# Performance work log

Measured on AMD Instinct MI355X. Metric: run time of the kernel, lower is better.

## Reference

```python
import jax, jax.numpy as jnp
import numpy as np

B, N, M = 512, 1024, 128
OUT_DIM, MOLVEC_DIM, IN_DIM = 256, 256, 512


def setup_inputs() -> dict:
    key = jax.random.key(0)
    ks = jax.random.split(key, 6)
    X = jax.random.normal(ks[0], (B, N, OUT_DIM), dtype=jnp.float32)
    molvec = jax.random.normal(ks[1], (B, MOLVEC_DIM), dtype=jnp.float32)
    idx_M = jax.random.randint(ks[2], (B, M), 0, N, dtype=jnp.int64)
    # Xavier-normal-ish scaled linear weights (torch layout: [out_features, in_features])
    fan_in1 = MOLVEC_DIM + OUT_DIM
    W1 = jax.random.normal(ks[3], (IN_DIM, fan_in1), dtype=jnp.float32) * jnp.sqrt(2.0 / (fan_in1 + IN_DIM))
    b1 = jnp.zeros((IN_DIM,), dtype=jnp.float32)
    W2 = jax.random.normal(ks[4], (IN_DIM, IN_DIM), dtype=jnp.float32) * jnp.sqrt(2.0 / (IN_DIM + IN_DIM))
    b2 = jnp.zeros((IN_DIM,), dtype=jnp.float32)
    return {"X": X, "molvec": molvec, "idx_M": idx_M, "W1": W1, "b1": b1, "W2": W2, "b2": b2}


def reference(X, molvec, idx_M, W1, b1, W2, b2):
    # Batched gather: replaces the per-sample index_select loop. [B, M, OUT_DIM]
    target_x = jnp.take_along_axis(X, idx_M[:, :, None], axis=1)
    # Broadcast molvec to each masked position and concat. [B, M, OUT_DIM+MOLVEC_DIM]
    mv = jnp.broadcast_to(molvec[:, None, :], (X.shape[0], idx_M.shape[1], molvec.shape[-1]))
    concat_x = jnp.concatenate([target_x, mv], axis=-1)
    # 2-layer MLP (fc1 -> relu -> fc2)
    h = jax.nn.relu(jnp.einsum('bmd,id->bmi', concat_x, W1) + b1)
    pred = jnp.einsum('bmi,oi->bmo', h, W2) + b2
    return pred.reshape(X.shape[0] * idx_M.shape[1], -1)
```

## Files before the change

kernel.cpp:

```cpp
#include <hip/hip_runtime.h>
#include <hip/hip_bf16.h>

#define BB 512
#define NN 1024
#define MM 128
#define OUTD 256
#define MOLD 256
#define IND 512
#define K1 512
#define RROWS 65536

typedef float f32x4 __attribute__((ext_vector_type(4)));
typedef short s16x8 __attribute__((ext_vector_type(8)));
typedef __bf16 bf16x8 __attribute__((ext_vector_type(8)));

#define AS_GLOBAL const __attribute__((address_space(1))) void
#define AS_LDS __attribute__((address_space(3))) void

__device__ __forceinline__ unsigned short f2bf(float f) {
    unsigned int u = __builtin_bit_cast(unsigned int, f);
    u = (u + 0x7fffu + ((u >> 16) & 1u)) >> 16;
    return (unsigned short)u;
}

__global__ __launch_bounds__(256) void prep_weights(
    const float* __restrict__ W1, const float* __restrict__ W2,
    unsigned short* __restrict__ W1b, unsigned short* __restrict__ W2b) {
    int i = blockIdx.x * 256 + threadIdx.x;
    float4 a = ((const float4*)W1)[i];
    ushort4 pa;
    pa.x = f2bf(a.x); pa.y = f2bf(a.y); pa.z = f2bf(a.z); pa.w = f2bf(a.w);
    ((ushort4*)W1b)[i] = pa;
    float4 b = ((const float4*)W2)[i];
    ushort4 pb;
    pb.x = f2bf(b.x); pb.y = f2bf(b.y); pb.z = f2bf(b.z); pb.w = f2bf(b.w);
    ((ushort4*)W2b)[i] = pb;
}

__global__ __launch_bounds__(256) void gemm1_kernel(
    const float* __restrict__ X, const float* __restrict__ mol,
    const int* __restrict__ idxp, const unsigned short* __restrict__ W1b,
    const float* __restrict__ b1, unsigned short* __restrict__ H) {
    __shared__ __align__(16) unsigned short Asm[128 * 32];
    __shared__ __align__(16) unsigned short Bsm[128 * 32];

    const int t = threadIdx.x;
    const int lane = t & 63, w = t >> 6;
    const int b = blockIdx.x;
    const int n0 = blockIdx.y * 128;
    const int wr = (w >> 1) * 64, wc = (w & 1) * 64;
    const int lr = lane & 15, quad = lane >> 4;

    const int arow = t >> 1;
    const int acol = (t & 1) * 16;
    const int idx = idxp[b * MM + arow];
    const float* Xrow = X + ((size_t)b * NN + idx) * OUTD;
    const float* mvrow = mol + (size_t)b * MOLD;

    f32x4 acc[4][4];
#pragma unroll
    for (int mi = 0; mi < 4; ++mi)
#pragma unroll
        for (int ni = 0; ni < 4; ++ni) acc[mi][ni] = {0.f, 0.f, 0.f, 0.f};

    for (int ki = 0; ki < 16; ++ki) {
        const int kt = ki * 32;
        const float* src = (kt < OUTD) ? (Xrow + kt + acol) : (mvrow + (kt - OUTD) + acol);
        const float4* s4 = (const float4*)src;
        float4 v0 = s4[0], v1 = s4[1], v2 = s4[2], v3 = s4[3];
        unsigned short* dst = &Asm[arow * 32 + acol];
        ushort4 p;
        p.x = f2bf(v0.x); p.y = f2bf(v0.y); p.z = f2bf(v0.z); p.w = f2bf(v0.w);
        *(ushort4*)(dst + 0) = p;
        p.x = f2bf(v1.x); p.y = f2bf(v1.y); p.z = f2bf(v1.z); p.w = f2bf(v1.w);
        *(ushort4*)(dst + 4) = p;
        p.x = f2bf(v2.x); p.y = f2bf(v2.y); p.z = f2bf(v2.z); p.w = f2bf(v2.w);
        *(ushort4*)(dst + 8) = p;
        p.x = f2bf(v3.x); p.y = f2bf(v3.y); p.z = f2bf(v3.z); p.w = f2bf(v3.w);
        *(ushort4*)(dst + 12) = p;
#pragma unroll
        for (int j = 0; j < 2; ++j) {
            const int cidx = j * 4 + w;
            const int s = cidx * 64 + lane;
            const unsigned short* gb = W1b + (size_t)(n0 + (s >> 2)) * K1 + kt + (s & 3) * 8;
            __builtin_amdgcn_global_load_lds((AS_GLOBAL*)gb, (AS_LDS*)(Bsm + cidx * 512), 16, 0, 0);
        }
        __syncthreads();
        s16x8 af[4], bfr[4];
#pragma unroll
        for (int i = 0; i < 4; ++i)
            af[i] = *(const s16x8*)&Asm[(wr + i * 16 + lr) * 32 + quad * 8];
#pragma unroll
        for (int i = 0; i < 4; ++i)
            bfr[i] = *(const s16x8*)&Bsm[(wc + i * 16 + lr) * 32 + quad * 8];
#pragma unroll
        for (int mi = 0; mi < 4; ++mi)
#pragma unroll
            for (int ni = 0; ni < 4; ++ni)
                acc[mi][ni] = __builtin_amdgcn_mfma_f32_16x16x32_bf16(
                    __builtin_bit_cast(bf16x8, af[mi]),
                    __builtin_bit_cast(bf16x8, bfr[ni]), acc[mi][ni], 0, 0, 0);
        __syncthreads();
    }

    float bias[4];
#pragma unroll
    for (int ni = 0; ni < 4; ++ni) bias[ni] = b1[n0 + wc + ni * 16 + lr];
    const int row0 = b * 128;
#pragma unroll
    for (int mi = 0; mi < 4; ++mi) {
#pragma unroll
        for (int ni = 0; ni < 4; ++ni) {
            const int gcol = n0 + wc + ni * 16 + lr;
#pragma unroll
            for (int rr = 0; rr < 4; ++rr) {
                const int grow = row0 + wr + mi * 16 + quad * 4 + rr;
                float v = acc[mi][ni][rr] + bias[ni];
                v = v > 0.f ? v : 0.f;
                H[(size_t)grow * IND + gcol] = f2bf(v);
            }
        }
    }
}

__global__ __launch_bounds__(256) void gemm2_kernel(
    const unsigned short* __restrict__ Hb, const unsigned short* __restrict__ W2b,
    const float* __restrict__ b2, float* __restrict__ out) {
    __shared__ __align__(16) unsigned short Asm[128 * 32];
    __shared__ __align__(16) unsigned short Bsm[128 * 32];

    const int t = threadIdx.x;
    const int lane = t & 63, w = t >> 6;
    const int row0 = blockIdx.x * 128;
    const int n0 = blockIdx.y * 128;
    const int wr = (w >> 1) * 64, wc = (w & 1) * 64;
    const int lr = lane & 15, quad = lane >> 4;

    f32x4 acc[4][4];
#pragma unroll
    for (int mi = 0; mi < 4; ++mi)
#pragma unroll
        for (int ni = 0; ni < 4; ++ni) acc[mi][ni] = {0.f, 0.f, 0.f, 0.f};

    for (int ki = 0; ki < 16; ++ki) {
        const int kt = ki * 32;
#pragma unroll
        for (int j = 0; j < 2; ++j) {
            const int cidx = j * 4 + w;
            const int s = cidx * 64 + lane;
            const unsigned short* ga = Hb + (size_t)(row0 + (s >> 2)) * IND + kt + (s & 3) * 8;
            __builtin_amdgcn_global_load_lds((AS_GLOBAL*)ga, (AS_LDS*)(Asm + cidx * 512), 16, 0, 0);
            const unsigned short* gb = W2b + (size_t)(n0 + (s >> 2)) * IND + kt + (s & 3) * 8;
            __builtin_amdgcn_global_load_lds((AS_GLOBAL*)gb, (AS_LDS*)(Bsm + cidx * 512), 16, 0, 0);
        }
        __syncthreads();
        s16x8 af[4], bfr[4];
#pragma unroll
        for (int i = 0; i < 4; ++i)
            af[i] = *(const s16x8*)&Asm[(wr + i * 16 + lr) * 32 + quad * 8];
#pragma unroll
        for (int i = 0; i < 4; ++i)
            bfr[i] = *(const s16x8*)&Bsm[(wc + i * 16 + lr) * 32 + quad * 8];
#pragma unroll
        for (int mi = 0; mi < 4; ++mi)
#pragma unroll
            for (int ni = 0; ni < 4; ++ni)
                acc[mi][ni] = __builtin_amdgcn_mfma_f32_16x16x32_bf16(
                    __builtin_bit_cast(bf16x8, af[mi]),
                    __builtin_bit_cast(bf16x8, bfr[ni]), acc[mi][ni], 0, 0, 0);
        __syncthreads();
    }

    float bias[4];
#pragma unroll
    for (int ni = 0; ni < 4; ++ni) bias[ni] = b2[n0 + wc + ni * 16 + lr];
#pragma unroll
    for (int mi = 0; mi < 4; ++mi) {
#pragma unroll
        for (int ni = 0; ni < 4; ++ni) {
            const int gcol = n0 + wc + ni * 16 + lr;
#pragma unroll
            for (int rr = 0; rr < 4; ++rr) {
                const int grow = row0 + wr + mi * 16 + quad * 4 + rr;
                out[(size_t)grow * IND + gcol] = acc[mi][ni][rr] + bias[ni];
            }
        }
    }
}

extern "C" void kernel_launch(void* const* d_in, const int* in_sizes, int n_in,
                              void* d_out, int out_size, void* d_ws, size_t ws_size,
                              hipStream_t stream) {
    const float* X = (const float*)d_in[0];
    const float* mol = (const float*)d_in[1];
    const int* idx = (const int*)d_in[2];
    const float* W1 = (const float*)d_in[3];
    const float* b1 = (const float*)d_in[4];
    const float* W2 = (const float*)d_in[5];
    const float* b2 = (const float*)d_in[6];
    float* out = (float*)d_out;

    unsigned short* W1b = (unsigned short*)d_ws;
    unsigned short* W2b = W1b + 512 * 512;
    unsigned short* H = W2b + 512 * 512;

    prep_weights<<<256, 256, 0, stream>>>(W1, W2, W1b, W2b);
    gemm1_kernel<<<dim3(BB, IND / 128), 256, 0, stream>>>(X, mol, idx, W1b, b1, H);
    gemm2_kernel<<<dim3(RROWS / 128, IND / 128), 256, 0, stream>>>(H, W2b, b2, out);
}
```

Before: 733.5 us.

## Precompute per-batch molvec contribution and pre-gather X rows to bf16

The molvec half of fc1 is the same for every masked position in a batch. It is now computed once per batch by a small fp32 kernel (C1 = W1_mol·molvec + b1) and used as a per-row bias, which halves the K dimension of gemm1. The X row gather and bf16 conversion move into a separate gather kernel, so gemm1 can stream A through global_load_lds like gemm2. The cost is two extra launches and a 32MB bf16 intermediate that is written and then read back.

```diff
diff --git a/kernel.cpp b/kernel.cpp
--- a/kernel.cpp
+++ b/kernel.cpp
@@ -7,7 +7,6 @@
 #define OUTD 256
 #define MOLD 256
 #define IND 512
-#define K1 512
 #define RROWS 65536
 
 typedef float f32x4 __attribute__((ext_vector_type(4)));
@@ -25,64 +24,93 @@
 
 __global__ __launch_bounds__(256) void prep_weights(
     const float* __restrict__ W1, const float* __restrict__ W2,
-    unsigned short* __restrict__ W1b, unsigned short* __restrict__ W2b) {
+    unsigned short* __restrict__ W1ab, unsigned short* __restrict__ W2b) {
     int i = blockIdx.x * 256 + threadIdx.x;
-    float4 a = ((const float4*)W1)[i];
-    ushort4 pa;
-    pa.x = f2bf(a.x); pa.y = f2bf(a.y); pa.z = f2bf(a.z); pa.w = f2bf(a.w);
-    ((ushort4*)W1b)[i] = pa;
     float4 b = ((const float4*)W2)[i];
     ushort4 pb;
     pb.x = f2bf(b.x); pb.y = f2bf(b.y); pb.z = f2bf(b.z); pb.w = f2bf(b.w);
     ((ushort4*)W2b)[i] = pb;
+    if (i < 32768) {
+        int row = i >> 6, c4 = i & 63;
+        float4 a = ((const float4*)(W1 + (size_t)row * 512))[c4];
+        ushort4 pa;
+        pa.x = f2bf(a.x); pa.y = f2bf(a.y); pa.z = f2bf(a.z); pa.w = f2bf(a.w);
+        ((ushort4*)(W1ab + (size_t)row * 256))[c4] = pa;
+    }
+}
+
+__global__ __launch_bounds__(256) void c1_kernel(
+    const float* __restrict__ mol, const float* __restrict__ W1,
+    const float* __restrict__ b1, float* __restrict__ C1) {
+    __shared__ float ms[MOLD];
+    const int b = blockIdx.x, t = threadIdx.x;
+    ms[t] = mol[(size_t)b * MOLD + t];
+    __syncthreads();
+#pragma unroll
+    for (int h = 0; h < 2; ++h) {
+        const int n = h * 256 + t;
+        const f32x4* w = (const f32x4*)(W1 + (size_t)n * 512 + 256);
+        float acc = 0.f;
+#pragma unroll 4
+        for (int k4 = 0; k4 < 64; ++k4) {
+            f32x4 wv = w[k4];
+            acc += wv[0] * ms[k4 * 4 + 0];
+            acc += wv[1] * ms[k4 * 4 + 1];
+            acc += wv[2] * ms[k4 * 4 + 2];
+            acc += wv[3] * ms[k4 * 4 + 3];
+        }
+        C1[(size_t)b * IND + n] = acc + b1[n];
+    }
+}
+
+__global__ __launch_bounds__(256) void gather_kernel(
+    const float* __restrict__ X, const int* __restrict__ idxp,
+    unsigned short* __restrict__ Ag) {
+    const int t = threadIdx.x;
+    const int r = blockIdx.x * 8 + (t >> 5);
+    const int l = t & 31;
+    const int b = r >> 7;
+    const int idx = idxp[r];
+    const float* src = X + ((size_t)b * NN + idx) * OUTD + l * 8;
+    float4 v0 = ((const float4*)src)[0];
+    float4 v1 = ((const float4*)src)[1];
+    ushort4 p0, p1;
+    p0.x = f2bf(v0.x); p0.y = f2bf(v0.y); p0.z = f2bf(v0.z); p0.w = f2bf(v0.w);
+    p1.x = f2bf(v1.x); p1.y = f2bf(v1.y); p1.z = f2bf(v1.z); p1.w = f2bf(v1.w);
+    unsigned short* dst = Ag + (size_t)r * OUTD + l * 8;
+    ((ushort4*)dst)[0] = p0;
+    ((ushort4*)dst)[1] = p1;
 }
 
 __global__ __launch_bounds__(256) void gemm1_kernel(
-    const float* __restrict__ X, const float* __restrict__ mol,
-    const int* __restrict__ idxp, const unsigned short* __restrict__ W1b,
-    const float* __restrict__ b1, unsigned short* __restrict__ H) {
+    const unsigned short* __restrict__ Ag, const unsigned short* __restrict__ W1ab,
+    const float* __restrict__ C1, unsigned short* __restrict__ H) {
     __shared__ __align__(16) unsigned short Asm[128 * 32];
     __shared__ __align__(16) unsigned short Bsm[128 * 32];
 
     const int t = threadIdx.x;
     const int lane = t & 63, w = t >> 6;
     const int b = blockIdx.x;
+    const int row0 = b * 128;
     const int n0 = blockIdx.y * 128;
     const int wr = (w >> 1) * 64, wc = (w & 1) * 64;
     const int lr = lane & 15, quad = lane >> 4;
 
-    const int arow = t >> 1;
-    const int acol = (t & 1) * 16;
-    const int idx = idxp[b * MM + arow];
-    const float* Xrow = X + ((size_t)b * NN + idx) * OUTD;
-    const float* mvrow = mol + (size_t)b * MOLD;
-
     f32x4 acc[4][4];
 #pragma unroll
     for (int mi = 0; mi < 4; ++mi)
 #pragma unroll
         for (int ni = 0; ni < 4; ++ni) acc[mi][ni] = {0.f, 0.f, 0.f, 0.f};
 
-    for (int ki = 0; ki < 16; ++ki) {
+    for (int ki = 0; ki < 8; ++ki) {
         const int kt = ki * 32;
-        const float* src = (kt < OUTD) ? (Xrow + kt + acol) : (mvrow + (kt - OUTD) + acol);
-        const float4* s4 = (const float4*)src;
-        float4 v0 = s4[0], v1 = s4[1], v2 = s4[2], v3 = s4[3];
-        unsigned short* dst = &Asm[arow * 32 + acol];
-        ushort4 p;
-        p.x = f2bf(v0.x); p.y = f2bf(v0.y); p.z = f2bf(v0.z); p.w = f2bf(v0.w);
-        *(ushort4*)(dst + 0) = p;
-        p.x = f2bf(v1.x); p.y = f2bf(v1.y); p.z = f2bf(v1.z); p.w = f2bf(v1.w);
-        *(ushort4*)(dst + 4) = p;
-        p.x = f2bf(v2.x); p.y = f2bf(v2.y); p.z = f2bf(v2.z); p.w = f2bf(v2.w);
-        *(ushort4*)(dst + 8) = p;
-        p.x = f2bf(v3.x); p.y = f2bf(v3.y); p.z = f2bf(v3.z); p.w = f2bf(v3.w);
-        *(ushort4*)(dst + 12) = p;
 #pragma unroll
         for (int j = 0; j < 2; ++j) {
             const int cidx = j * 4 + w;
             const int s = cidx * 64 + lane;
-            const unsigned short* gb = W1b + (size_t)(n0 + (s >> 2)) * K1 + kt + (s & 3) * 8;
+            const unsigned short* ga = Ag + (size_t)(row0 + (s >> 2)) * OUTD + kt + (s & 3) * 8;
+            __builtin_amdgcn_global_load_lds((AS_GLOBAL*)ga, (AS_LDS*)(Asm + cidx * 512), 16, 0, 0);
+            const unsigned short* gb = W1ab + (size_t)(n0 + (s >> 2)) * OUTD + kt + (s & 3) * 8;
             __builtin_amdgcn_global_load_lds((AS_GLOBAL*)gb, (AS_LDS*)(Bsm + cidx * 512), 16, 0, 0);
         }
         __syncthreads();
@@ -105,8 +133,7 @@
 
     float bias[4];
 #pragma unroll
-    for (int ni = 0; ni < 4; ++ni) bias[ni] = b1[n0 + wc + ni * 16 + lr];
-    const int row0 = b * 128;
+    for (int ni = 0; ni < 4; ++ni) bias[ni] = C1[(size_t)b * IND + n0 + wc + ni * 16 + lr];
 #pragma unroll
     for (int mi = 0; mi < 4; ++mi) {
 #pragma unroll
@@ -200,11 +227,15 @@
     const float* b2 = (const float*)d_in[6];
     float* out = (float*)d_out;
 
-    unsigned short* W1b = (unsigned short*)d_ws;
-    unsigned short* W2b = W1b + 512 * 512;
-    unsigned short* H = W2b + 512 * 512;
-
-    prep_weights<<<256, 256, 0, stream>>>(W1, W2, W1b, W2b);
-    gemm1_kernel<<<dim3(BB, IND / 128), 256, 0, stream>>>(X, mol, idx, W1b, b1, H);
+    unsigned short* W1ab = (unsigned short*)d_ws;
+    unsigned short* W2b = W1ab + 512 * 256;
+    float* C1 = (float*)(W2b + 512 * 512);
+    unsigned short* Ag = (unsigned short*)(C1 + 512 * 512);
+    unsigned short* H = Ag + (size_t)RROWS * OUTD;
+
+    prep_weights<<<256, 256, 0, stream>>>(W1, W2, W1ab, W2b);
+    c1_kernel<<<512, 256, 0, stream>>>(mol, W1, b1, C1);
+    gather_kernel<<<8192, 256, 0, stream>>>(X, idx, Ag);
+    gemm1_kernel<<<dim3(BB, IND / 128), 256, 0, stream>>>(Ag, W1ab, C1, H);
     gemm2_kernel<<<dim3(RROWS / 128, IND / 128), 256, 0, stream>>>(H, W2b, b2, out);
 }
```

Measured after the change: 741.5 us. No clear change (+1.1%).
